# Kernel tuning notes

Hardware: AMD Instinct MI355X
Metric: run time of the kernel (lower is better)

## Reference

```python
import jax, jax.numpy as jnp
import numpy as np

N = 8192
D_IN = 32
HIDDEN = [32, 32, 32]   # -> 2 GraphConvolution layers
FC = [32, 1]            # hfc = [32, 32, 1] -> 2 Linear layers


def _uniform(key, shape, stdv):
    return jax.random.uniform(key, shape, jnp.float32, -stdv, stdv)


def setup_inputs() -> dict:
    key = jax.random.key(0)
    ks = jax.random.split(key, 32)
    inp = {}
    inp["V"] = jax.random.normal(ks[0], (N, D_IN), jnp.float32)
    inp["adj"] = jax.random.randint(ks[1], (N, N), 0, 4, jnp.int32)
    # GCN layer params: w1, w2, w3 [in, out], bias [out]; init U(-stdv, stdv), stdv = 1/sqrt(out)
    ki = 2
    for li in range(len(HIDDEN) - 1):
        a, b = HIDDEN[li], HIDDEN[li + 1]
        stdv = 1.0 / np.sqrt(b)
        for wname in ("w1", "w2", "w3"):
            inp[f"{wname}_{li}"] = _uniform(ks[ki], (a, b), stdv); ki += 1
        inp[f"gb_{li}"] = _uniform(ks[ki], (b,), stdv); ki += 1
    # FC params (torch Linear default init: U(-1/sqrt(in), 1/sqrt(in)))
    hfc = [HIDDEN[-1]] + FC
    for li in range(len(hfc) - 1):
        a, b = hfc[li], hfc[li + 1]
        stdv = 1.0 / np.sqrt(a)
        inp[f"fcW_{li}"] = _uniform(ks[ki], (b, a), stdv); ki += 1  # torch Linear weight is [out, in]
        inp[f"fcb_{li}"] = _uniform(ks[ki], (b,), stdv); ki += 1
    return inp


def _gcn(V, adj, w1, w2, w3, bias):
    # masked-adjacency relational aggregation: sum_k (adj==k) @ (V @ w_k)
    dt = V.dtype
    o = (adj == 1).astype(dt) @ (V @ w1)
    o = o + (adj == 2).astype(dt) @ (V @ w2)
    o = o + (adj == 3).astype(dt) @ (V @ w3)
    return jax.nn.relu(o + bias)


def reference(V, adj, w1_0, w2_0, w3_0, gb_0, w1_1, w2_1, w3_1, gb_1,
              fcW_0, fcb_0, fcW_1, fcb_1):
    Z = _gcn(V, adj, w1_0, w2_0, w3_0, gb_0)          # [N, 32]
    Z = _gcn(Z, adj, w1_1, w2_1, w3_1, gb_1)          # [N, 32]
    Z = jnp.sum(Z, axis=0)                             # [32] sum pooling over nodes
    Z = jax.nn.relu(Z @ fcW_0.T + fcb_0)               # dropout = identity (eval mode)
    Z = Z @ fcW_1.T + fcb_1                            # [1]
    return jax.nn.sigmoid(Z)
```

## Files before the change

### kernel.cpp

```cpp
#include <hip/hip_runtime.h>
#include <cmath>

#define NN 8192

typedef _Float16 half8 __attribute__((ext_vector_type(8)));
typedef float floatx4 __attribute__((ext_vector_type(4)));
typedef unsigned int uint;

template <int L2>
__global__ __launch_bounds__(256) void h_kernel(
    const float* __restrict__ X, const float* __restrict__ w1,
    const float* __restrict__ w2, const float* __restrict__ w3,
    const float* __restrict__ gbias, _Float16* __restrict__ Hfrag) {
  __shared__ float wl[32][32];
  __shared__ float Xs[64][32];
  const int tid = threadIdx.x;
  const int ch = blockIdx.y;
  const float* wsrc = (ch == 0) ? w1 : (ch == 1) ? w2 : w3;
  for (int i = tid; i < 1024; i += 256) ((float*)wl)[i] = wsrc[i];
  const size_t base = (size_t)blockIdx.x * 2048 + tid * 8;
  if (L2 == 0) {
    float4 x0 = ((const float4*)(X + base))[0];
    float4 x1 = ((const float4*)(X + base))[1];
    *((float4*)(&Xs[0][0] + tid * 8)) = x0;
    *((float4*)(&Xs[0][0] + tid * 8 + 4)) = x1;
  } else {
    float4 s0 = {0.f, 0.f, 0.f, 0.f}, s1 = {0.f, 0.f, 0.f, 0.f};
#pragma unroll
    for (int c = 0; c < 8; ++c) {
      const float4* p = (const float4*)(X + (size_t)c * NN * 32 + base);
      float4 a = p[0], b = p[1];
      s0.x += a.x; s0.y += a.y; s0.z += a.z; s0.w += a.w;
      s1.x += b.x; s1.y += b.y; s1.z += b.z; s1.w += b.w;
    }
    const int c0 = (tid * 8) & 31;
    const float4 b0 = *(const float4*)(gbias + c0);
    const float4 b1 = *(const float4*)(gbias + c0 + 4);
    s0.x += b0.x; s0.y += b0.y; s0.z += b0.z; s0.w += b0.w;
    s1.x += b1.x; s1.y += b1.y; s1.z += b1.z; s1.w += b1.w;
    s0.x = s0.x > 0.f ? s0.x : 0.f; s0.y = s0.y > 0.f ? s0.y : 0.f;
    s0.z = s0.z > 0.f ? s0.z : 0.f; s0.w = s0.w > 0.f ? s0.w : 0.f;
    s1.x = s1.x > 0.f ? s1.x : 0.f; s1.y = s1.y > 0.f ? s1.y : 0.f;
    s1.z = s1.z > 0.f ? s1.z : 0.f; s1.w = s1.w > 0.f ? s1.w : 0.f;
    *((float4*)(&Xs[0][0] + tid * 8)) = s0;
    *((float4*)(&Xs[0][0] + tid * 8 + 4)) = s1;
  }
  __syncthreads();
  const int n = tid & 31, jb = tid >> 5;
  const int j0 = blockIdx.x * 64 + jb * 8;
  const int t = j0 >> 5;
  const int lane = (n & 15) | (((j0 & 31) >> 3) << 4);
  const int tile = n >> 4;
  half8 hv;
#pragma unroll
  for (int jj = 0; jj < 8; ++jj) {
    const float4* xr = (const float4*)(&Xs[jb * 8 + jj][0]);
    float acc = 0.f;
#pragma unroll
    for (int d4 = 0; d4 < 8; ++d4) {
      float4 x = xr[d4];
      acc += x.x * wl[d4 * 4 + 0][n];
      acc += x.y * wl[d4 * 4 + 1][n];
      acc += x.z * wl[d4 * 4 + 2][n];
      acc += x.w * wl[d4 * 4 + 3][n];
    }
    hv[jj] = (_Float16)acc;
  }
  size_t idx = ((((size_t)ch * 256 + t) * 2 + tile) * 64 + lane) * 8;
  *(half8*)(Hfrag + idx) = hv;
}

__global__ __launch_bounds__(256, 8) void pack_kernel(
    const int* __restrict__ adj, uint* __restrict__ packed_g) {
  __shared__ uint ptile[2048];
  const int tid = threadIdx.x;
  const int rg = blockIdx.x >> 3, c = blockIdx.x & 7;
  const int tg = tid >> 5;
  const int qt = (tid >> 1) & 3;
  const int t4 = (tid >> 3) & 3;
  const int ih = tid & 1;
  const int byte_base = tg * 1024 + qt * 256 + t4 * 4 + ih;
  unsigned char* pb = (unsigned char*)ptile;
  const size_t gofs = (size_t)rg * 32 * NN + c * 1024 + tid * 4;
#pragma unroll 4
  for (int r = 0; r < 32; ++r) {
    int4 a = *(const int4*)(adj + gofs + (size_t)r * NN);
    const uint b = (uint)(a.x & 3) | ((uint)(a.y & 3) << 2) |
                   ((uint)(a.z & 3) << 4) | ((uint)(a.w & 3) << 6);
    pb[byte_base + (r & 15) * 16 + (r >> 4) * 2] = (unsigned char)b;
  }
  __syncthreads();
  uint* pg = packed_g + (size_t)blockIdx.x * 2048;
  *(uint4*)(pg + tid * 8) = *(const uint4*)(ptile + tid * 8);
  *(uint4*)(pg + tid * 8 + 4) = *(const uint4*)(ptile + tid * 8 + 4);
}

__device__ __forceinline__ void agg_phaseB(const uint* ptile, float* red_raw,
                                           const half8* __restrict__ Hf,
                                           float* __restrict__ Zpart, int rg,
                                           int c, int tid) {
  const int w = tid >> 6, lane = tid & 63;
  const int m = lane & 15, q = lane >> 4;
  uint mk[8];
  *(uint4*)(mk) = *(const uint4*)(ptile + (w * 2) * 256 + lane * 4);
  *(uint4*)(mk + 4) = *(const uint4*)(ptile + (w * 2 + 1) * 256 + lane * 4);
  __syncthreads();
  floatx4 acc00 = {0.f, 0.f, 0.f, 0.f}, acc01 = {0.f, 0.f, 0.f, 0.f};
  floatx4 acc10 = {0.f, 0.f, 0.f, 0.f}, acc11 = {0.f, 0.f, 0.f, 0.f};
#pragma unroll 2
  for (int tl = 0; tl < 8; ++tl) {
    const int t = c * 32 + w * 8 + tl;
    const size_t hb = (size_t)t * 128 + lane;
    half8 b00 = Hf[hb],          b01 = Hf[hb + 64];
    half8 b10 = Hf[hb + 32768],  b11 = Hf[hb + 32768 + 64];
    half8 b20 = Hf[hb + 65536],  b21 = Hf[hb + 65536 + 64];
    const uint pk = mk[tl];
    half8 a1r0, a2r0, a3r0, a1r1, a2r1, a3r1;
#pragma unroll
    for (int i = 0; i < 8; ++i) {
      const int p0 = (pk >> (2 * i)) & 3;
      const int p1 = (pk >> (16 + 2 * i)) & 3;
      a1r0[i] = (p0 == 1) ? (_Float16)1.f : (_Float16)0.f;
      a2r0[i] = (p0 == 2) ? (_Float16)1.f : (_Float16)0.f;
      a3r0[i] = (p0 == 3) ? (_Float16)1.f : (_Float16)0.f;
      a1r1[i] = (p1 == 1) ? (_Float16)1.f : (_Float16)0.f;
      a2r1[i] = (p1 == 2) ? (_Float16)1.f : (_Float16)0.f;
      a3r1[i] = (p1 == 3) ? (_Float16)1.f : (_Float16)0.f;
    }
    acc00 = __builtin_amdgcn_mfma_f32_16x16x32_f16(a1r0, b00, acc00, 0, 0, 0);
    acc00 = __builtin_amdgcn_mfma_f32_16x16x32_f16(a2r0, b10, acc00, 0, 0, 0);
    acc00 = __builtin_amdgcn_mfma_f32_16x16x32_f16(a3r0, b20, acc00, 0, 0, 0);
    acc01 = __builtin_amdgcn_mfma_f32_16x16x32_f16(a1r0, b01, acc01, 0, 0, 0);
    acc01 = __builtin_amdgcn_mfma_f32_16x16x32_f16(a2r0, b11, acc01, 0, 0, 0);
    acc01 = __builtin_amdgcn_mfma_f32_16x16x32_f16(a3r0, b21, acc01, 0, 0, 0);
    acc10 = __builtin_amdgcn_mfma_f32_16x16x32_f16(a1r1, b00, acc10, 0, 0, 0);
    acc10 = __builtin_amdgcn_mfma_f32_16x16x32_f16(a2r1, b10, acc10, 0, 0, 0);
    acc10 = __builtin_amdgcn_mfma_f32_16x16x32_f16(a3r1, b20, acc10, 0, 0, 0);
    acc11 = __builtin_amdgcn_mfma_f32_16x16x32_f16(a1r1, b01, acc11, 0, 0, 0);
    acc11 = __builtin_amdgcn_mfma_f32_16x16x32_f16(a2r1, b11, acc11, 0, 0, 0);
    acc11 = __builtin_amdgcn_mfma_f32_16x16x32_f16(a3r1, b21, acc11, 0, 0, 0);
  }
  float (*red)[4][64][4] = (float (*)[4][64][4])red_raw;
#pragma unroll
  for (int r = 0; r < 4; ++r) {
    red[w][0][lane][r] = acc00[r];
    red[w][1][lane][r] = acc01[r];
    red[w][2][lane][r] = acc10[r];
    red[w][3][lane][r] = acc11[r];
  }
  __syncthreads();
  if (w == 0) {
    const int rbase = rg * 32;
#pragma unroll
    for (int r = 0; r < 4; ++r) {
      const float c00 = red[0][0][lane][r] + red[1][0][lane][r] +
                        red[2][0][lane][r] + red[3][0][lane][r];
      const float c01 = red[0][1][lane][r] + red[1][1][lane][r] +
                        red[2][1][lane][r] + red[3][1][lane][r];
      const float c10 = red[0][2][lane][r] + red[1][2][lane][r] +
                        red[2][2][lane][r] + red[3][2][lane][r];
      const float c11 = red[0][3][lane][r] + red[1][3][lane][r] +
                        red[2][3][lane][r] + red[3][3][lane][r];
      const int ro0 = rbase + q * 4 + r;
      float* zp0 = Zpart + ((size_t)c * NN + ro0) * 32;
      zp0[m] = c00;
      zp0[16 + m] = c01;
      float* zp1 = Zpart + ((size_t)c * NN + ro0 + 16) * 32;
      zp1[m] = c10;
      zp1[16 + m] = c11;
    }
  }
}

__global__ __launch_bounds__(256, 8) void agg_kernel(
    const uint* __restrict__ packed_g, const half8* __restrict__ Hf,
    float* __restrict__ Zpart) {
  __shared__ char smraw[16384];
  uint* ptile = (uint*)smraw;
  const int tid = threadIdx.x;
  const int rg = blockIdx.x >> 3, c = blockIdx.x & 7;
  const uint* pg = packed_g + (size_t)blockIdx.x * 2048;
  uint4 u0 = *(const uint4*)(pg + tid * 8);
  uint4 u1 = *(const uint4*)(pg + tid * 8 + 4);
  *(uint4*)(ptile + tid * 8) = u0;
  *(uint4*)(ptile + tid * 8 + 4) = u1;
  __syncthreads();
  agg_phaseB(ptile, (float*)smraw, Hf, Zpart, rg, c, tid);
}

__global__ __launch_bounds__(256) void pool_kernel(
    const float* __restrict__ Zpart, const float* __restrict__ bias,
    float* __restrict__ partials) {
  const int tid = threadIdx.x;
  const int col = tid & 31, ro = tid >> 5;
  const float b = bias[col];
  float s = 0.f;
  for (int rr = 0; rr < 32; ++rr) {
    const size_t r = (size_t)blockIdx.x * 256 + ro * 32 + rr;
    float v = b;
#pragma unroll
    for (int c = 0; c < 8; ++c) v += Zpart[(size_t)c * NN * 32 + r * 32 + col];
    s += v > 0.f ? v : 0.f;
  }
  __shared__ float red[8][32];
  red[ro][col] = s;
  __syncthreads();
  if (tid < 32) {
    float t = 0.f;
#pragma unroll
    for (int i = 0; i < 8; ++i) t += red[i][tid];
    partials[(size_t)blockIdx.x * 32 + tid] = t;
  }
}

__global__ __launch_bounds__(256) void fc_kernel(
    const float* __restrict__ partials, int np, const float* __restrict__ W0,
    const float* __restrict__ b0, const float* __restrict__ W1,
    const float* __restrict__ b1, float* __restrict__ out) {
  __shared__ float acc8[8][32];
  __shared__ float z[32], y[32];
  const int tid = threadIdx.x;
  const int col = tid & 31, ch = tid >> 5;
  float s = 0.f;
  for (int i = ch; i < np; i += 8) s += partials[(size_t)i * 32 + col];
  acc8[ch][col] = s;
  __syncthreads();
  if (tid < 32) {
    float t = 0.f;
#pragma unroll
    for (int i = 0; i < 8; ++i) t += acc8[i][tid];
    z[tid] = t;
  }
  __syncthreads();
  if (tid < 32) {
    float acc = b0[tid];
    for (int n = 0; n < 32; ++n) acc += W0[tid * 32 + n] * z[n];
    y[tid] = acc > 0.f ? acc : 0.f;
  }
  __syncthreads();
  if (tid == 0) {
    float acc = b1[0];
    for (int mm = 0; mm < 32; ++mm) acc += W1[mm] * y[mm];
    out[0] = 1.f / (1.f + expf(-acc));
  }
}

extern "C" void kernel_launch(void* const* d_in, const int* in_sizes, int n_in,
                              void* d_out, int out_size, void* d_ws,
                              size_t ws_size, hipStream_t stream) {
  const float* V   = (const float*)d_in[0];
  const int*   adj = (const int*)d_in[1];
  const float *w10 = (const float*)d_in[2], *w20 = (const float*)d_in[3],
              *w30 = (const float*)d_in[4], *gb0 = (const float*)d_in[5];
  const float *w11 = (const float*)d_in[6], *w21 = (const float*)d_in[7],
              *w31 = (const float*)d_in[8], *gb1 = (const float*)d_in[9];
  const float *fW0 = (const float*)d_in[10], *fb0 = (const float*)d_in[11],
              *fW1 = (const float*)d_in[12], *fb1 = (const float*)d_in[13];
  float* out = (float*)d_out;
  char* ws = (char*)d_ws;

  _Float16* Hfrag    = (_Float16*)ws;
  float*    Zpart    = (float*)(ws + 1572864);
  float*    partials = (float*)(ws + 9961472);
  uint*     packed   = (uint*)(ws + 10223616);

  pack_kernel<<<2048, 256, 0, stream>>>(adj, packed);
  h_kernel<0><<<dim3(128, 3), 256, 0, stream>>>(V, w10, w20, w30, nullptr,
                                                Hfrag);
  agg_kernel<<<2048, 256, 0, stream>>>(packed, (const half8*)Hfrag, Zpart);
  h_kernel<1><<<dim3(128, 3), 256, 0, stream>>>(Zpart, w11, w21, w31, gb0,
                                                Hfrag);
  agg_kernel<<<2048, 256, 0, stream>>>(packed, (const half8*)Hfrag, Zpart);
  pool_kernel<<<32, 256, 0, stream>>>(Zpart, gb1, partials);
  fc_kernel<<<1, 256, 0, stream>>>(partials, 32, fW0, fb0, fW1, fb1, out);
}
```

Before: 468.0 us.

## Pack adjacency row-major and read masks directly from global in aggregation

The pack kernel now writes the 2-bit adjacency codes in plain row-major order, one thread per output word, with no shared-memory tile or barrier. The aggregation kernel drops its shared staging of the packed tile and loads 16-bit mask fragments straight from global memory for each row and k-step. This removes one shared round-trip and a sync per block, at the cost of small, strided 2-byte global loads inside the MFMA loop. Those loads may be less coalesced than the old uint4 staging.

```diff
diff --git a/kernel.cpp b/kernel.cpp
--- a/kernel.cpp
+++ b/kernel.cpp
@@ -70,62 +70,60 @@
   *(half8*)(Hfrag + idx) = hv;
 }
 
-__global__ __launch_bounds__(256, 8) void pack_kernel(
+__global__ __launch_bounds__(256) void pack_kernel(
     const int* __restrict__ adj, uint* __restrict__ packed_g) {
-  __shared__ uint ptile[2048];
-  const int tid = threadIdx.x;
-  const int rg = blockIdx.x >> 3, c = blockIdx.x & 7;
-  const int tg = tid >> 5;
-  const int qt = (tid >> 1) & 3;
-  const int t4 = (tid >> 3) & 3;
-  const int ih = tid & 1;
-  const int byte_base = tg * 1024 + qt * 256 + t4 * 4 + ih;
-  unsigned char* pb = (unsigned char*)ptile;
-  const size_t gofs = (size_t)rg * 32 * NN + c * 1024 + tid * 4;
-#pragma unroll 4
-  for (int r = 0; r < 32; ++r) {
-    int4 a = *(const int4*)(adj + gofs + (size_t)r * NN);
-    const uint b = (uint)(a.x & 3) | ((uint)(a.y & 3) << 2) |
-                   ((uint)(a.z & 3) << 4) | ((uint)(a.w & 3) << 6);
-    pb[byte_base + (r & 15) * 16 + (r >> 4) * 2] = (unsigned char)b;
-  }
-  __syncthreads();
-  uint* pg = packed_g + (size_t)blockIdx.x * 2048;
-  *(uint4*)(pg + tid * 8) = *(const uint4*)(ptile + tid * 8);
-  *(uint4*)(pg + tid * 8 + 4) = *(const uint4*)(ptile + tid * 8 + 4);
-}
-
-__device__ __forceinline__ void agg_phaseB(const uint* ptile, float* red_raw,
-                                           const half8* __restrict__ Hf,
-                                           float* __restrict__ Zpart, int rg,
-                                           int c, int tid) {
+  const uint gid = blockIdx.x * 256 + threadIdx.x;
+#pragma unroll 2
+  for (int it = 0; it < 8; ++it) {
+    const size_t widx = (size_t)it * 524288 + gid;
+    const int4* ap = (const int4*)(adj + widx * 16);
+    uint word = 0;
+#pragma unroll
+    for (int k = 0; k < 4; ++k) {
+      int4 a = ap[k];
+      const uint b = (uint)(a.x & 3) | ((uint)(a.y & 3) << 2) |
+                     ((uint)(a.z & 3) << 4) | ((uint)(a.w & 3) << 6);
+      word |= b << (8 * k);
+    }
+    packed_g[widx] = word;
+  }
+}
+
+__global__ __launch_bounds__(256, 8) void agg_kernel(
+    const unsigned char* __restrict__ packed_b, const half8* __restrict__ Hf,
+    float* __restrict__ Zpart) {
+  const int tid = threadIdx.x;
   const int w = tid >> 6, lane = tid & 63;
   const int m = lane & 15, q = lane >> 4;
-  uint mk[8];
-  *(uint4*)(mk) = *(const uint4*)(ptile + (w * 2) * 256 + lane * 4);
-  *(uint4*)(mk + 4) = *(const uint4*)(ptile + (w * 2 + 1) * 256 + lane * 4);
-  __syncthreads();
+  const int rg = blockIdx.x >> 3, c = blockIdx.x & 7;
+  const int rbase = rg * 32;
+  const int row0 = rbase + m, row1 = row0 + 16;
+  const unsigned char* p0 =
+      packed_b + (size_t)row0 * 2048 + c * 256 + w * 64 + q * 2;
+  const unsigned char* p1 =
+      packed_b + (size_t)row1 * 2048 + c * 256 + w * 64 + q * 2;
   floatx4 acc00 = {0.f, 0.f, 0.f, 0.f}, acc01 = {0.f, 0.f, 0.f, 0.f};
   floatx4 acc10 = {0.f, 0.f, 0.f, 0.f}, acc11 = {0.f, 0.f, 0.f, 0.f};
 #pragma unroll 2
   for (int tl = 0; tl < 8; ++tl) {
     const int t = c * 32 + w * 8 + tl;
+    const uint pk0 = *(const unsigned short*)(p0 + tl * 8);
+    const uint pk1 = *(const unsigned short*)(p1 + tl * 8);
     const size_t hb = (size_t)t * 128 + lane;
     half8 b00 = Hf[hb],          b01 = Hf[hb + 64];
     half8 b10 = Hf[hb + 32768],  b11 = Hf[hb + 32768 + 64];
     half8 b20 = Hf[hb + 65536],  b21 = Hf[hb + 65536 + 64];
-    const uint pk = mk[tl];
     half8 a1r0, a2r0, a3r0, a1r1, a2r1, a3r1;
 #pragma unroll
     for (int i = 0; i < 8; ++i) {
-      const int p0 = (pk >> (2 * i)) & 3;
-      const int p1 = (pk >> (16 + 2 * i)) & 3;
-      a1r0[i] = (p0 == 1) ? (_Float16)1.f : (_Float16)0.f;
-      a2r0[i] = (p0 == 2) ? (_Float16)1.f : (_Float16)0.f;
-      a3r0[i] = (p0 == 3) ? (_Float16)1.f : (_Float16)0.f;
-      a1r1[i] = (p1 == 1) ? (_Float16)1.f : (_Float16)0.f;
-      a2r1[i] = (p1 == 2) ? (_Float16)1.f : (_Float16)0.f;
-      a3r1[i] = (p1 == 3) ? (_Float16)1.f : (_Float16)0.f;
+      const int v0 = (pk0 >> (2 * i)) & 3;
+      const int v1 = (pk1 >> (2 * i)) & 3;
+      a1r0[i] = (v0 == 1) ? (_Float16)1.f : (_Float16)0.f;
+      a2r0[i] = (v0 == 2) ? (_Float16)1.f : (_Float16)0.f;
+      a3r0[i] = (v0 == 3) ? (_Float16)1.f : (_Float16)0.f;
+      a1r1[i] = (v1 == 1) ? (_Float16)1.f : (_Float16)0.f;
+      a2r1[i] = (v1 == 2) ? (_Float16)1.f : (_Float16)0.f;
+      a3r1[i] = (v1 == 3) ? (_Float16)1.f : (_Float16)0.f;
     }
     acc00 = __builtin_amdgcn_mfma_f32_16x16x32_f16(a1r0, b00, acc00, 0, 0, 0);
     acc00 = __builtin_amdgcn_mfma_f32_16x16x32_f16(a2r0, b10, acc00, 0, 0, 0);
@@ -140,7 +138,7 @@
     acc11 = __builtin_amdgcn_mfma_f32_16x16x32_f16(a2r1, b11, acc11, 0, 0, 0);
     acc11 = __builtin_amdgcn_mfma_f32_16x16x32_f16(a3r1, b21, acc11, 0, 0, 0);
   }
-  float (*red)[4][64][4] = (float (*)[4][64][4])red_raw;
+  __shared__ float red[4][4][64][4];
 #pragma unroll
   for (int r = 0; r < 4; ++r) {
     red[w][0][lane][r] = acc00[r];
@@ -150,7 +148,6 @@
   }
   __syncthreads();
   if (w == 0) {
-    const int rbase = rg * 32;
 #pragma unroll
     for (int r = 0; r < 4; ++r) {
       const float c00 = red[0][0][lane][r] + red[1][0][lane][r] +
@@ -172,22 +169,6 @@
   }
 }
 
-__global__ __launch_bounds__(256, 8) void agg_kernel(
-    const uint* __restrict__ packed_g, const half8* __restrict__ Hf,
-    float* __restrict__ Zpart) {
-  __shared__ char smraw[16384];
-  uint* ptile = (uint*)smraw;
-  const int tid = threadIdx.x;
-  const int rg = blockIdx.x >> 3, c = blockIdx.x & 7;
-  const uint* pg = packed_g + (size_t)blockIdx.x * 2048;
-  uint4 u0 = *(const uint4*)(pg + tid * 8);
-  uint4 u1 = *(const uint4*)(pg + tid * 8 + 4);
-  *(uint4*)(ptile + tid * 8) = u0;
-  *(uint4*)(ptile + tid * 8 + 4) = u1;
-  __syncthreads();
-  agg_phaseB(ptile, (float*)smraw, Hf, Zpart, rg, c, tid);
-}
-
 __global__ __launch_bounds__(256) void pool_kernel(
     const float* __restrict__ Zpart, const float* __restrict__ bias,
     float* __restrict__ partials) {
@@ -267,10 +248,12 @@
   pack_kernel<<<2048, 256, 0, stream>>>(adj, packed);
   h_kernel<0><<<dim3(128, 3), 256, 0, stream>>>(V, w10, w20, w30, nullptr,
                                                 Hfrag);
-  agg_kernel<<<2048, 256, 0, stream>>>(packed, (const half8*)Hfrag, Zpart);
+  agg_kernel<<<2048, 256, 0, stream>>>((const unsigned char*)packed,
+                                       (const half8*)Hfrag, Zpart);
   h_kernel<1><<<dim3(128, 3), 256, 0, stream>>>(Zpart, w11, w21, w31, gb0,
                                                 Hfrag);
-  agg_kernel<<<2048, 256, 0, stream>>>(packed, (const half8*)Hfrag, Zpart);
+  agg_kernel<<<2048, 256, 0, stream>>>((const unsigned char*)packed,
+                                       (const half8*)Hfrag, Zpart);
   pool_kernel<<<32, 256, 0, stream>>>(Zpart, gb1, partials);
   fc_kernel<<<1, 256, 0, stream>>>(partials, 32, fW0, fb0, fW1, fb1, out);
 }
```

Measured after the change: 469.1 us. About the same (+0.2%).
